# Kernel tuning notes

Hardware: AMD Instinct MI355X
Metric: run time of the kernel (lower is better)

## Reference

```python
import jax, jax.numpy as jnp
import numpy as np

E = 8        # num_experts
C = 1024     # n_emb
H = 4096     # n_emb * ff_mult
B, T = 4, 1024


def setup_inputs() -> dict:
    key = jax.random.key(0)
    k_x, k_g, k_1, k_2, k_3 = jax.random.split(key, 5)
    scale = 0.02
    return {
        "x": jax.random.normal(k_x, (B, T, C), dtype=jnp.float32),
        "Wg": jax.random.normal(k_g, (E, C), dtype=jnp.float32) * scale,   # gate: Linear(C, E), weight [E, C]
        "W1": jax.random.normal(k_1, (E, C, H), dtype=jnp.float32) * scale,  # per-expert w1 (transposed for einsum)
        "W2": jax.random.normal(k_2, (E, H, C), dtype=jnp.float32) * scale,  # per-expert w2
        "W3": jax.random.normal(k_3, (E, C, H), dtype=jnp.float32) * scale,  # per-expert w3
        "top_k": 2,
    }


def reference(x, Wg, W1, W2, W3, top_k):
    Bd, Td, Cd = x.shape
    xf = x.reshape(-1, Cd)                                   # [N, C]
    N = xf.shape[0]
    logits = jnp.einsum('nc,ec->ne', xf, Wg)                 # router logits [N, E]
    probs = jax.nn.softmax(logits.astype(jnp.float32), axis=-1)
    w, sel = jax.lax.top_k(probs, top_k)                     # [N, k]
    w = w / w.sum(axis=-1, keepdims=True)                    # renormalize over selected
    # combine weight per (token, expert): sum of normalized topk weights routed to e
    cw = jnp.zeros((N, E), jnp.float32).at[jnp.arange(N)[:, None], sel].add(w)
    # dense grouped SwiGLU over all experts; combine weights zero out unselected experts
    h1 = jnp.einsum('nc,ech->neh', xf, W1)                   # [N, E, H]
    g = jax.nn.silu(h1) * jnp.einsum('nc,ech->neh', xf, W3)  # [N, E, H]
    out = jnp.einsum('neh,ehc,ne->nc', g, W2, cw.astype(x.dtype))
    return out.reshape(Bd, Td, Cd)
```

## Files before the change

kernel.cpp:

```cpp
#include <hip/hip_runtime.h>
#include <hip/hip_bf16.h>

#define E_     8
#define C_     1024
#define H_     4096
#define N_TOK  4096
#define TOPK   2
#define NSLOT  (N_TOK*TOPK)
#define SPAD   (NSLOT+256)

#define LPAD 40

typedef __attribute__((ext_vector_type(4))) float f32x4;
typedef __attribute__((ext_vector_type(8))) short short8;

__device__ __forceinline__ unsigned short f2bf(float f) {
    return __builtin_bit_cast(unsigned short, __float2bfloat16(f));
}

__device__ __forceinline__ void gload16(const void* g, const void* l) {
    __builtin_amdgcn_global_load_lds(
        (const __attribute__((address_space(1))) unsigned int*)g,
        (__attribute__((address_space(3))) unsigned int*)l, 16, 0, 0);
}

#define WAITVM_(n) asm volatile("s_waitcnt vmcnt(" #n ")" ::: "memory")
#define WAITVM(n) WAITVM_(n)

__global__ void router_kernel(const float* __restrict__ x, const float* __restrict__ Wg,
                              int* __restrict__ sel, float* __restrict__ wts) {
    int wave = (blockIdx.x * blockDim.x + threadIdx.x) >> 6;
    int lane = threadIdx.x & 63;
    if (wave >= N_TOK) return;
    const float* xr = x + (size_t)wave * C_;
    float acc[E_];
#pragma unroll
    for (int e = 0; e < E_; ++e) acc[e] = 0.f;
    for (int c = lane; c < C_; c += 64) {
        float xv = xr[c];
#pragma unroll
        for (int e = 0; e < E_; ++e) acc[e] += xv * Wg[e * C_ + c];
    }
#pragma unroll
    for (int e = 0; e < E_; ++e) {
#pragma unroll
        for (int off = 32; off > 0; off >>= 1) acc[e] += __shfl_xor(acc[e], off);
    }
    if (lane == 0) {
        float mx = acc[0];
#pragma unroll
        for (int e = 1; e < E_; ++e) mx = fmaxf(mx, acc[e]);
        float p[E_]; float s = 0.f;
#pragma unroll
        for (int e = 0; e < E_; ++e) { p[e] = __expf(acc[e] - mx); s += p[e]; }
        float inv = 1.f / s;
#pragma unroll
        for (int e = 0; e < E_; ++e) p[e] *= inv;
        int b0 = 0; float v0 = p[0];
#pragma unroll
        for (int e = 1; e < E_; ++e) if (p[e] > v0) { v0 = p[e]; b0 = e; }
        int b1 = -1; float v1 = -1.f;
#pragma unroll
        for (int e = 0; e < E_; ++e) { if (e != b0 && p[e] > v1) { v1 = p[e]; b1 = e; } }
        float isum = 1.f / (v0 + v1);
        sel[wave*2]   = b0; sel[wave*2+1] = b1;
        wts[wave*2]   = v0 * isum; wts[wave*2+1] = v1 * isum;
    }
}

__global__ void assign_kernel(const int* __restrict__ sel, const float* __restrict__ wts,
                              int* __restrict__ counts, int* __restrict__ offsets,
                              int* __restrict__ pos_of_slot, int* __restrict__ token_of,
                              float* __restrict__ slotw) {
    __shared__ int cnt[256][E_];
    __shared__ int offs[E_];
    int t = threadIdx.x;
    const int PER = NSLOT / 256;
    int base = t * PER;
    int loc[E_];
#pragma unroll
    for (int e = 0; e < E_; ++e) loc[e] = 0;
    for (int i = 0; i < PER; ++i) loc[sel[base + i]]++;
#pragma unroll
    for (int e = 0; e < E_; ++e) cnt[t][e] = loc[e];
    __syncthreads();
    if (t < E_) {
        int run = 0;
        for (int i = 0; i < 256; ++i) { int c = cnt[i][t]; cnt[i][t] = run; run += c; }
        counts[t] = run;
    }
    __syncthreads();
    if (t == 0) {
        int s = 0;
        for (int e = 0; e < E_; ++e) { offs[e] = s; offsets[e] = s; s += counts[e]; }
    }
    __syncthreads();
    int run[E_];
#pragma unroll
    for (int e = 0; e < E_; ++e) run[e] = offs[e] + cnt[t][e];
    for (int i = 0; i < PER; ++i) {
        int s = base + i;
        int e = sel[s];
        int p = run[e]++;
        pos_of_slot[s] = p;
        token_of[p] = s >> 1;
        slotw[p] = wts[s];
    }
}

__global__ void copy_kernel(const float* __restrict__ x, const int* __restrict__ pos_of_slot,
                            unsigned short* __restrict__ Xg) {
    int slot = blockIdx.x * 4 + (threadIdx.x >> 6);
    int lane = threadIdx.x & 63;
    int pos = pos_of_slot[slot];
    int n = slot >> 1;
    const float* xr = x + (size_t)n * C_;
    unsigned short* dst = Xg + (size_t)pos * C_;
#pragma unroll
    for (int i = 0; i < 4; ++i) {
        int c0 = i * 256 + lane * 4;
        float4 v = *(const float4*)(xr + c0);
        ushort4 b;
        b.x = f2bf(v.x); b.y = f2bf(v.y); b.z = f2bf(v.z); b.w = f2bf(v.w);
        *(ushort4*)(dst + c0) = b;
    }
}

__global__ void wconv_kernel(const float* __restrict__ src, unsigned short* __restrict__ dst,
                             int R, int Cc) {
    int e = blockIdx.z;
    int c0 = blockIdx.x * 64;
    int r0 = blockIdx.y * 64;
    const float* s = src + (size_t)e * R * Cc;
    unsigned short* d = dst + (size_t)e * R * Cc;
    __shared__ unsigned short t_[64][72];
    int t = threadIdx.x;
    int tr = t >> 4, tc4 = (t & 15) * 4;
#pragma unroll
    for (int i = 0; i < 4; ++i) {
        int r = tr + i * 16;
        float4 v = *(const float4*)(s + (size_t)(r0 + r) * Cc + c0 + tc4);
        t_[r][tc4+0] = f2bf(v.x); t_[r][tc4+1] = f2bf(v.y);
        t_[r][tc4+2] = f2bf(v.z); t_[r][tc4+3] = f2bf(v.w);
    }
    __syncthreads();
    int oc = t >> 2, seg = (t & 3) * 16;
    short8 w0, w1;
#pragma unroll
    for (int j = 0; j < 8; ++j) {
        w0[j] = (short)t_[seg + j][oc];
        w1[j] = (short)t_[seg + 8 + j][oc];
    }
    unsigned short* dp = d + (size_t)(c0 + oc) * R + r0 + seg;
    *(short8*)dp = w0;
    *(short8*)(dp + 8) = w1;
}


#define G1_NH (C_/32)

__global__ __launch_bounds__(512, 2) void gemm1_ring(
        const unsigned short* __restrict__ Xg, const unsigned short* __restrict__ W1t,
        const unsigned short* __restrict__ W3t, unsigned short* __restrict__ G,
        const int* __restrict__ counts, const int* __restrict__ offsets) {
    int b = blockIdx.y * 32 + blockIdx.x;
    int e = b & 7;
    int j = b >> 3;
    int ct = j & 31;
    int rt = j >> 5;
    int ne = counts[e];
    if (rt * 256 >= ne) return;
    int row0 = offsets[e] + rt * 256;
    int n0 = ct * 128;

    extern __shared__ char lds[];
    char* As  = lds;
    char* B1s = lds + 65536;
    char* B3s = lds + 98304;

    int tid = threadIdx.x, lane = tid & 63, wid = tid >> 6;
    int wm = wid >> 1, wn = wid & 1;
    int fr = lane & 15, q = lane >> 4;
    int arow = lane & 15, akch = lane >> 4;

    const unsigned short* Ap  = Xg + (size_t)row0 * C_;
    const unsigned short* B1p = W1t + ((size_t)e * H_ + n0) * C_;
    const unsigned short* B3p = W3t + ((size_t)e * H_ + n0) * C_;

    f32x4 acc1[4][4], acc3[4][4];
#pragma unroll
    for (int m = 0; m < 4; ++m)
#pragma unroll
        for (int n = 0; n < 4; ++n) {
            acc1[m][n] = (f32x4){0.f,0.f,0.f,0.f};
            acc3[m][n] = (f32x4){0.f,0.f,0.f,0.f};
        }

    auto STAGE_A = [&](int hs, int slot) {
        int k0 = hs * 32;
#pragma unroll
        for (int jj = 0; jj < 2; ++jj) {
            int g = wid + jj * 8;
            gload16(Ap + (size_t)(g * 16 + arow) * C_ + k0 + akch * 8,
                    As + slot * 16384 + g * 1024);
        }
    };
    auto STAGE_B = [&](int hs, int slot) {
        int k0 = hs * 32;
        gload16(B1p + (size_t)(wid * 16 + arow) * C_ + k0 + akch * 8,
                B1s + slot * 8192 + wid * 1024);
        gload16(B3p + (size_t)(wid * 16 + arow) * C_ + k0 + akch * 8,
                B3s + slot * 8192 + wid * 1024);
    };

    STAGE_A(0, 0); STAGE_B(0, 0);
    STAGE_A(1, 1); STAGE_B(1, 1);
    STAGE_A(2, 2); STAGE_B(2, 2);
    WAITVM(8);
    __builtin_amdgcn_s_barrier();

    for (int h = 0; h < G1_NH; ++h) {
        int slot = h & 3;
        int hs = (h + 3 < G1_NH) ? h + 3 : G1_NH - 1;
        int wslot = (h + 3) & 3;
        short8 a[4], b1[4], b3[4];
#pragma unroll
        for (int m = 0; m < 4; ++m)
            a[m] = *(const short8*)(As + slot * 16384 + (wm * 4 + m) * 1024 + q * 256 + fr * 16);
#pragma unroll
        for (int n = 0; n < 4; ++n)
            b1[n] = *(const short8*)(B1s + slot * 8192 + (wn * 4 + n) * 1024 + q * 256 + fr * 16);
        STAGE_A(hs, wslot);
        __builtin_amdgcn_sched_barrier(0);
        __builtin_amdgcn_s_barrier();
        __builtin_amdgcn_s_setprio(1);
#pragma unroll
        for (int m = 0; m < 4; ++m)
#pragma unroll
            for (int n = 0; n < 4; ++n)
                acc1[m][n] = __builtin_amdgcn_mfma_f32_16x16x32_bf16(a[m], b1[n], acc1[m][n], 0, 0, 0);
        __builtin_amdgcn_s_setprio(0);
        __builtin_amdgcn_s_barrier();
#pragma unroll
        for (int n = 0; n < 4; ++n)
            b3[n] = *(const short8*)(B3s + slot * 8192 + (wn * 4 + n) * 1024 + q * 256 + fr * 16);
        STAGE_B(hs, wslot);
        WAITVM(8);
        __builtin_amdgcn_sched_barrier(0);
        __builtin_amdgcn_s_barrier();
        __builtin_amdgcn_s_setprio(1);
#pragma unroll
        for (int m = 0; m < 4; ++m)
#pragma unroll
            for (int n = 0; n < 4; ++n)
                acc3[m][n] = __builtin_amdgcn_mfma_f32_16x16x32_bf16(a[m], b3[n], acc3[m][n], 0, 0, 0);
        __builtin_amdgcn_s_setprio(0);
        __builtin_amdgcn_s_barrier();
    }
    WAITVM(0);

#pragma unroll
    for (int m = 0; m < 4; ++m)
#pragma unroll
        for (int rg = 0; rg < 4; ++rg) {
            int row = wm*64 + m*16 + q*4 + rg;
            if (rt * 256 + row < ne) {
                size_t gbase = (size_t)(row0 + row) * H_ + n0 + wn*64;
#pragma unroll
                for (int n = 0; n < 4; ++n) {
                    float h1 = acc1[m][n][rg];
                    float h3 = acc3[m][n][rg];
                    float g = h1 * h3 / (1.f + __expf(-h1));
                    G[gbase + n*16 + fr] = f2bf(g);
                }
            }
        }
}

#define G2_NH (H_/32)

__global__ __launch_bounds__(512, 2) void gemm2_ring(
        const unsigned short* __restrict__ G, const unsigned short* __restrict__ W2t,
        float* __restrict__ out, const int* __restrict__ counts,
        const int* __restrict__ offsets, const int* __restrict__ token_of,
        const float* __restrict__ slotw) {
    int b = blockIdx.y * 8 + blockIdx.x;
    int e = b & 7;
    int j = b >> 3;
    int ct = j & 7;
    int rt = j >> 3;
    int ne = counts[e];
    if (rt * 256 >= ne) return;
    int row0 = offsets[e] + rt * 256;
    int n0 = ct * 128;

    extern __shared__ char lds[];
    char* As = lds;
    char* Bs = lds + 98304;

    int tid = threadIdx.x, lane = tid & 63, wid = tid >> 6;
    int wm = wid >> 1, wn = wid & 1;
    int fr = lane & 15, q = lane >> 4;
    int arow = lane & 15, akch = lane >> 4;

    const unsigned short* Ap = G + (size_t)row0 * H_;
    const unsigned short* Bp = W2t + ((size_t)e * C_ + n0) * H_;

    f32x4 acc[4][4];
#pragma unroll
    for (int m = 0; m < 4; ++m)
#pragma unroll
        for (int n = 0; n < 4; ++n) acc[m][n] = (f32x4){0.f,0.f,0.f,0.f};

    auto STAGE = [&](int hs, int slot) {
        int k0 = hs * 32;
#pragma unroll
        for (int jj = 0; jj < 2; ++jj) {
            int g = wid + jj * 8;
            gload16(Ap + (size_t)(g * 16 + arow) * H_ + k0 + akch * 8,
                    As + slot * 16384 + g * 1024);
        }
        gload16(Bp + (size_t)(wid * 16 + arow) * H_ + k0 + akch * 8,
                Bs + slot * 8192 + wid * 1024);
    };

    STAGE(0, 0); STAGE(1, 1); STAGE(2, 2); STAGE(3, 3); STAGE(4, 4);
    WAITVM(12);
    __builtin_amdgcn_s_barrier();

    int slot = 0, wslot = 5;
    for (int h = 0; h < G2_NH; ++h) {
        int hs = (h + 5 < G2_NH) ? h + 5 : G2_NH - 1;
        short8 a[4], bfr[4];
#pragma unroll
        for (int m = 0; m < 4; ++m)
            a[m] = *(const short8*)(As + slot * 16384 + (wm * 4 + m) * 1024 + q * 256 + fr * 16);
#pragma unroll
        for (int n = 0; n < 4; ++n)
            bfr[n] = *(const short8*)(Bs + slot * 8192 + (wn * 4 + n) * 1024 + q * 256 + fr * 16);
        STAGE(hs, wslot);
        WAITVM(12);
        __builtin_amdgcn_sched_barrier(0);
        __builtin_amdgcn_s_barrier();
        __builtin_amdgcn_s_setprio(1);
#pragma unroll
        for (int m = 0; m < 4; ++m)
#pragma unroll
            for (int n = 0; n < 4; ++n)
                acc[m][n] = __builtin_amdgcn_mfma_f32_16x16x32_bf16(a[m], bfr[n], acc[m][n], 0, 0, 0);
        __builtin_amdgcn_s_setprio(0);
        __builtin_amdgcn_s_barrier();
        slot = (slot == 5) ? 0 : slot + 1;
        wslot = (wslot == 5) ? 0 : wslot + 1;
    }
    WAITVM(0);

#pragma unroll
    for (int m = 0; m < 4; ++m)
#pragma unroll
        for (int rg = 0; rg < 4; ++rg) {
            int row = wm*64 + m*16 + q*4 + rg;
            if (rt * 256 + row < ne) {
                int grow = row0 + row;
                int tok = token_of[grow];
                float w = slotw[grow];
                float* orow = out + (size_t)tok * C_ + n0 + wn*64;
#pragma unroll
                for (int n = 0; n < 4; ++n)
                    atomicAdd(orow + n*16 + fr, acc[m][n][rg] * w);
            }
        }
}

#define BM 128
#define BN 128
#define BK 32
__global__ __launch_bounds__(256, 2) void gemm1_slow(
        const unsigned short* __restrict__ Xg, const float* __restrict__ W1,
        const float* __restrict__ W3, unsigned short* __restrict__ G,
        const int* __restrict__ counts, const int* __restrict__ offsets) {
    int ct = blockIdx.x;
    int rslot = blockIdx.y;
    int e = rslot >> 5, rt = rslot & 31;
    int ne = counts[e];
    if (rt * BM >= ne) return;
    int row0 = offsets[e] + rt * BM;
    int n0 = ct * BN;

    __shared__ unsigned short As[BM][LPAD];
    __shared__ unsigned short B1s[BN][LPAD];
    __shared__ unsigned short B3s[BN][LPAD];

    int tid = threadIdx.x;
    int lane = tid & 63, wid = tid >> 6;
    int wr = (wid >> 1) * 64, wc = (wid & 1) * 64;

    f32x4 acc1[4][4], acc3[4][4];
#pragma unroll
    for (int m = 0; m < 4; ++m)
#pragma unroll
        for (int n = 0; n < 4; ++n) {
            acc1[m][n] = (f32x4){0.f,0.f,0.f,0.f};
            acc3[m][n] = (f32x4){0.f,0.f,0.f,0.f};
        }

    const float* B1p = W1 + (size_t)e * C_ * H_ + n0;
    const float* B3p = W3 + (size_t)e * C_ * H_ + n0;
    int chunk = tid & 3, rr = tid >> 2;
    int kq = tid >> 5, n4 = tid & 31;

    for (int k0 = 0; k0 < C_; k0 += BK) {
        __syncthreads();
#pragma unroll
        for (int h = 0; h < 2; ++h) {
            int row = rr + h * 64;
            uint4 v = *(const uint4*)(Xg + (size_t)(row0 + row) * C_ + k0 + chunk * 8);
            *(uint4*)&As[row][chunk * 8] = v;
        }
        {
            float4 r0 = *(const float4*)(B1p + (size_t)(k0 + kq*4 + 0) * H_ + n4*4);
            float4 r1 = *(const float4*)(B1p + (size_t)(k0 + kq*4 + 1) * H_ + n4*4);
            float4 r2 = *(const float4*)(B1p + (size_t)(k0 + kq*4 + 2) * H_ + n4*4);
            float4 r3 = *(const float4*)(B1p + (size_t)(k0 + kq*4 + 3) * H_ + n4*4);
            ushort4 w0 = {f2bf(r0.x), f2bf(r1.x), f2bf(r2.x), f2bf(r3.x)};
            ushort4 w1 = {f2bf(r0.y), f2bf(r1.y), f2bf(r2.y), f2bf(r3.y)};
            ushort4 w2 = {f2bf(r0.z), f2bf(r1.z), f2bf(r2.z), f2bf(r3.z)};
            ushort4 w3 = {f2bf(r0.w), f2bf(r1.w), f2bf(r2.w), f2bf(r3.w)};
            *(ushort4*)&B1s[n4*4+0][kq*4] = w0;
            *(ushort4*)&B1s[n4*4+1][kq*4] = w1;
            *(ushort4*)&B1s[n4*4+2][kq*4] = w2;
            *(ushort4*)&B1s[n4*4+3][kq*4] = w3;
            r0 = *(const float4*)(B3p + (size_t)(k0 + kq*4 + 0) * H_ + n4*4);
            r1 = *(const float4*)(B3p + (size_t)(k0 + kq*4 + 1) * H_ + n4*4);
            r2 = *(const float4*)(B3p + (size_t)(k0 + kq*4 + 2) * H_ + n4*4);
            r3 = *(const float4*)(B3p + (size_t)(k0 + kq*4 + 3) * H_ + n4*4);
            w0 = (ushort4){f2bf(r0.x), f2bf(r1.x), f2bf(r2.x), f2bf(r3.x)};
            w1 = (ushort4){f2bf(r0.y), f2bf(r1.y), f2bf(r2.y), f2bf(r3.y)};
            w2 = (ushort4){f2bf(r0.z), f2bf(r1.z), f2bf(r2.z), f2bf(r3.z)};
            w3 = (ushort4){f2bf(r0.w), f2bf(r1.w), f2bf(r2.w), f2bf(r3.w)};
            *(ushort4*)&B3s[n4*4+0][kq*4] = w0;
            *(ushort4*)&B3s[n4*4+1][kq*4] = w1;
            *(ushort4*)&B3s[n4*4+2][kq*4] = w2;
            *(ushort4*)&B3s[n4*4+3][kq*4] = w3;
        }
        __syncthreads();
        int q = lane >> 4, fr = lane & 15;
        short8 a[4], b1[4], b3[4];
#pragma unroll
        for (int m = 0; m < 4; ++m) a[m] = *(const short8*)&As[wr + m*16 + fr][q*8];
#pragma unroll
        for (int n = 0; n < 4; ++n) {
            b1[n] = *(const short8*)&B1s[wc + n*16 + fr][q*8];
            b3[n] = *(const short8*)&B3s[wc + n*16 + fr][q*8];
        }
#pragma unroll
        for (int m = 0; m < 4; ++m)
#pragma unroll
            for (int n = 0; n < 4; ++n) {
                acc1[m][n] = __builtin_amdgcn_mfma_f32_16x16x32_bf16(a[m], b1[n], acc1[m][n], 0, 0, 0);
                acc3[m][n] = __builtin_amdgcn_mfma_f32_16x16x32_bf16(a[m], b3[n], acc3[m][n], 0, 0, 0);
            }
    }
    int q = lane >> 4, cfr = lane & 15;
#pragma unroll
    for (int m = 0; m < 4; ++m) {
#pragma unroll
        for (int rg = 0; rg < 4; ++rg) {
            int row = wr + m*16 + q*4 + rg;
            if (rt * BM + row < ne) {
                size_t gbase = (size_t)(row0 + row) * H_ + n0;
#pragma unroll
                for (int n = 0; n < 4; ++n) {
                    float h1 = acc1[m][n][rg];
                    float h3 = acc3[m][n][rg];
                    float g = h1 * h3 / (1.f + __expf(-h1));
                    G[gbase + wc + n*16 + cfr] = f2bf(g);
                }
            }
        }
    }
}

__global__ __launch_bounds__(256, 2) void gemm2_slow(
        const unsigned short* __restrict__ G, const float* __restrict__ W2,
        float* __restrict__ out, const int* __restrict__ counts,
        const int* __restrict__ offsets, const int* __restrict__ token_of,
        const float* __restrict__ slotw) {
    int ct = blockIdx.x;
    int rslot = blockIdx.y;
    int e = rslot >> 5, rt = rslot & 31;
    int ne = counts[e];
    if (rt * BM >= ne) return;
    int row0 = offsets[e] + rt * BM;
    int n0 = ct * BN;

    __shared__ unsigned short As[BM][LPAD];
    __shared__ unsigned short Bs[BN][LPAD];

    int tid = threadIdx.x;
    int lane = tid & 63, wid = tid >> 6;
    int wr = (wid >> 1) * 64, wc = (wid & 1) * 64;

    f32x4 acc[4][4];
#pragma unroll
    for (int m = 0; m < 4; ++m)
#pragma unroll
        for (int n = 0; n < 4; ++n) acc[m][n] = (f32x4){0.f,0.f,0.f,0.f};

    const float* Bp = W2 + (size_t)e * H_ * C_ + n0;
    int chunk = tid & 3, rr = tid >> 2;
    int kq = tid >> 5, n4 = tid & 31;

    for (int k0 = 0; k0 < H_; k0 += BK) {
        __syncthreads();
#pragma unroll
        for (int h = 0; h < 2; ++h) {
            int row = rr + h * 64;
            uint4 v = *(const uint4*)(G + (size_t)(row0 + row) * H_ + k0 + chunk * 8);
            *(uint4*)&As[row][chunk * 8] = v;
        }
        {
            float4 r0 = *(const float4*)(Bp + (size_t)(k0 + kq*4 + 0) * C_ + n4*4);
            float4 r1 = *(const float4*)(Bp + (size_t)(k0 + kq*4 + 1) * C_ + n4*4);
            float4 r2 = *(const float4*)(Bp + (size_t)(k0 + kq*4 + 2) * C_ + n4*4);
            float4 r3 = *(const float4*)(Bp + (size_t)(k0 + kq*4 + 3) * C_ + n4*4);
            ushort4 w0 = {f2bf(r0.x), f2bf(r1.x), f2bf(r2.x), f2bf(r3.x)};
            ushort4 w1 = {f2bf(r0.y), f2bf(r1.y), f2bf(r2.y), f2bf(r3.y)};
            ushort4 w2 = {f2bf(r0.z), f2bf(r1.z), f2bf(r2.z), f2bf(r3.z)};
            ushort4 w3 = {f2bf(r0.w), f2bf(r1.w), f2bf(r2.w), f2bf(r3.w)};
            *(ushort4*)&Bs[n4*4+0][kq*4] = w0;
            *(ushort4*)&Bs[n4*4+1][kq*4] = w1;
            *(ushort4*)&Bs[n4*4+2][kq*4] = w2;
            *(ushort4*)&Bs[n4*4+3][kq*4] = w3;
        }
        __syncthreads();
        int q = lane >> 4, fr = lane & 15;
        short8 a[4], b[4];
#pragma unroll
        for (int m = 0; m < 4; ++m) a[m] = *(const short8*)&As[wr + m*16 + fr][q*8];
#pragma unroll
        for (int n = 0; n < 4; ++n) b[n] = *(const short8*)&Bs[wc + n*16 + fr][q*8];
#pragma unroll
        for (int m = 0; m < 4; ++m)
#pragma unroll
            for (int n = 0; n < 4; ++n)
                acc[m][n] = __builtin_amdgcn_mfma_f32_16x16x32_bf16(a[m], b[n], acc[m][n], 0, 0, 0);
    }
    int q = lane >> 4, cfr = lane & 15;
#pragma unroll
    for (int m = 0; m < 4; ++m) {
#pragma unroll
        for (int rg = 0; rg < 4; ++rg) {
            int row = wr + m*16 + q*4 + rg;
            if (rt * BM + row < ne) {
                int grow = row0 + row;
                int tok = token_of[grow];
                float w = slotw[grow];
                float* orow = out + (size_t)tok * C_ + n0;
#pragma unroll
                for (int n = 0; n < 4; ++n)
                    atomicAdd(orow + wc + n*16 + cfr, acc[m][n][rg] * w);
            }
        }
    }
}

extern "C" void kernel_launch(void* const* d_in, const int* in_sizes, int n_in,
                              void* d_out, int out_size, void* d_ws, size_t ws_size,
                              hipStream_t stream) {
    const float* x  = (const float*)d_in[0];
    const float* Wg = (const float*)d_in[1];
    const float* W1 = (const float*)d_in[2];
    const float* W2 = (const float*)d_in[3];
    const float* W3 = (const float*)d_in[4];
    float* out = (float*)d_out;

    char* ws = (char*)d_ws;
    size_t o = 0;
    int*   sel      = (int*)(ws + o);  o += (size_t)NSLOT * 4;
    float* wts      = (float*)(ws + o); o += (size_t)NSLOT * 4;
    int*   pos      = (int*)(ws + o);  o += (size_t)NSLOT * 4;
    int*   token_of = (int*)(ws + o);  o += (size_t)NSLOT * 4;
    float* slotw    = (float*)(ws + o); o += (size_t)NSLOT * 4;
    int*   counts   = (int*)(ws + o);
    int*   offsets  = counts + E_;     o += 256;
    unsigned short* Xg = (unsigned short*)(ws + o); o += (size_t)SPAD * C_ * 2;
    unsigned short* G  = (unsigned short*)(ws + o); o += (size_t)SPAD * H_ * 2;
    size_t need_slow = o;
    unsigned short* W1t = (unsigned short*)(ws + o); o += (size_t)E_ * H_ * C_ * 2;
    unsigned short* W3t = (unsigned short*)(ws + o); o += (size_t)E_ * H_ * C_ * 2;
    unsigned short* W2t = W1t;
    size_t need_fast = o;

    hipMemsetAsync(d_out, 0, (size_t)out_size * sizeof(float), stream);
    if (ws_size < need_slow) return;

    router_kernel<<<N_TOK/4, 256, 0, stream>>>(x, Wg, sel, wts);
    assign_kernel<<<1, 256, 0, stream>>>(sel, wts, counts, offsets, pos, token_of, slotw);
    copy_kernel<<<NSLOT/4, 256, 0, stream>>>(x, pos, Xg);

    if (ws_size >= need_fast) {
        hipFuncSetAttribute((const void*)gemm1_ring, hipFuncAttributeMaxDynamicSharedMemorySize, 131072);
        hipFuncSetAttribute((const void*)gemm2_ring, hipFuncAttributeMaxDynamicSharedMemorySize, 147456);
        wconv_kernel<<<dim3(H_/64, C_/64, E_), 256, 0, stream>>>(W1, W1t, C_, H_);
        wconv_kernel<<<dim3(H_/64, C_/64, E_), 256, 0, stream>>>(W3, W3t, C_, H_);
        gemm1_ring<<<dim3(H_/128, E_*32), 512, 131072, stream>>>(Xg, W1t, W3t, G, counts, offsets);
        wconv_kernel<<<dim3(C_/64, H_/64, E_), 256, 0, stream>>>(W2, W2t, H_, C_);
        gemm2_ring<<<dim3(C_/128, E_*32), 512, 147456, stream>>>(G, W2t, out, counts, offsets, token_of, slotw);
    } else {
        gemm1_slow<<<dim3(H_/BN, E_*32), 256, 0, stream>>>(Xg, W1, W3, G, counts, offsets);
        gemm2_slow<<<dim3(C_/BN, E_*32), 256, 0, stream>>>(G, W2, out, counts, offsets, token_of, slotw);
    }
}
```

Measured before the change: 594.4 us.

## Shrink expert GEMM tiles to 128x128 with 256 threads and shorter LDS rings

Both grouped expert GEMMs move from 256-row tiles with 512 threads to 128-row tiles with 256 threads (4 waves), which cuts LDS use and should let more blocks fit per CU. gemm1 merges its separate W1 and W3 stages into one stage per k-step with a 3-slot ring, and gemm2 shrinks from a 6-slot to a 4-slot ring. The aim is better occupancy and less padding waste on uneven per-expert token counts, at the cost of loading each weight tile twice as often and issuing more blocks.

```diff
diff --git a/kernel.cpp b/kernel.cpp
--- a/kernel.cpp
+++ b/kernel.cpp
@@ -159,7 +159,7 @@
 
 #define G1_NH (C_/32)
 
-__global__ __launch_bounds__(512, 2) void gemm1_ring(
+__global__ __launch_bounds__(256, 2) void gemm1_ring(
         const unsigned short* __restrict__ Xg, const unsigned short* __restrict__ W1t,
         const unsigned short* __restrict__ W3t, unsigned short* __restrict__ G,
         const int* __restrict__ counts, const int* __restrict__ offsets) {
@@ -169,14 +169,14 @@
     int ct = j & 31;
     int rt = j >> 5;
     int ne = counts[e];
-    if (rt * 256 >= ne) return;
-    int row0 = offsets[e] + rt * 256;
+    if (rt * 128 >= ne) return;
+    int row0 = offsets[e] + rt * 128;
     int n0 = ct * 128;
 
     extern __shared__ char lds[];
     char* As  = lds;
-    char* B1s = lds + 65536;
-    char* B3s = lds + 98304;
+    char* B1s = lds + 24576;
+    char* B3s = lds + 49152;
 
     int tid = threadIdx.x, lane = tid & 63, wid = tid >> 6;
     int wm = wid >> 1, wn = wid & 1;
@@ -196,66 +196,51 @@
             acc3[m][n] = (f32x4){0.f,0.f,0.f,0.f};
         }
 
-    auto STAGE_A = [&](int hs, int slot) {
+    auto STAGE = [&](int hs, int slot) {
         int k0 = hs * 32;
 #pragma unroll
         for (int jj = 0; jj < 2; ++jj) {
-            int g = wid + jj * 8;
-            gload16(Ap + (size_t)(g * 16 + arow) * C_ + k0 + akch * 8,
-                    As + slot * 16384 + g * 1024);
+            int g = wid + jj * 4;
+            gload16(Ap  + (size_t)(g * 16 + arow) * C_ + k0 + akch * 8,
+                    As  + slot * 8192 + g * 1024);
+            gload16(B1p + (size_t)(g * 16 + arow) * C_ + k0 + akch * 8,
+                    B1s + slot * 8192 + g * 1024);
+            gload16(B3p + (size_t)(g * 16 + arow) * C_ + k0 + akch * 8,
+                    B3s + slot * 8192 + g * 1024);
         }
     };
-    auto STAGE_B = [&](int hs, int slot) {
-        int k0 = hs * 32;
-        gload16(B1p + (size_t)(wid * 16 + arow) * C_ + k0 + akch * 8,
-                B1s + slot * 8192 + wid * 1024);
-        gload16(B3p + (size_t)(wid * 16 + arow) * C_ + k0 + akch * 8,
-                B3s + slot * 8192 + wid * 1024);
-    };
-
-    STAGE_A(0, 0); STAGE_B(0, 0);
-    STAGE_A(1, 1); STAGE_B(1, 1);
-    STAGE_A(2, 2); STAGE_B(2, 2);
-    WAITVM(8);
+
+    STAGE(0, 0); STAGE(1, 1);
+    WAITVM(6);
     __builtin_amdgcn_s_barrier();
 
     for (int h = 0; h < G1_NH; ++h) {
-        int slot = h & 3;
-        int hs = (h + 3 < G1_NH) ? h + 3 : G1_NH - 1;
-        int wslot = (h + 3) & 3;
+        int slot = h % 3;
+        int hs = (h + 2 < G1_NH) ? h + 2 : G1_NH - 1;
+        int wslot = (h + 2) % 3;
         short8 a[4], b1[4], b3[4];
 #pragma unroll
         for (int m = 0; m < 4; ++m)
-            a[m] = *(const short8*)(As + slot * 16384 + (wm * 4 + m) * 1024 + q * 256 + fr * 16);
-#pragma unroll
-        for (int n = 0; n < 4; ++n)
+            a[m] = *(const short8*)(As + slot * 8192 + (wm * 4 + m) * 1024 + q * 256 + fr * 16);
+#pragma unroll
+        for (int n = 0; n < 4; ++n) {
             b1[n] = *(const short8*)(B1s + slot * 8192 + (wn * 4 + n) * 1024 + q * 256 + fr * 16);
-        STAGE_A(hs, wslot);
+            b3[n] = *(const short8*)(B3s + slot * 8192 + (wn * 4 + n) * 1024 + q * 256 + fr * 16);
+        }
+        STAGE(hs, wslot);
+        WAITVM(6);
         __builtin_amdgcn_sched_barrier(0);
         __builtin_amdgcn_s_barrier();
         __builtin_amdgcn_s_setprio(1);
 #pragma unroll
         for (int m = 0; m < 4; ++m)
 #pragma unroll
-            for (int n = 0; n < 4; ++n)
+            for (int n = 0; n < 4; ++n) {
                 acc1[m][n] = __builtin_amdgcn_mfma_f32_16x16x32_bf16(a[m], b1[n], acc1[m][n], 0, 0, 0);
+                acc3[m][n] = __builtin_amdgcn_mfma_f32_16x16x32_bf16(a[m], b3[n], acc3[m][n], 0, 0, 0);
+            }
         __builtin_amdgcn_s_setprio(0);
         __builtin_amdgcn_s_barrier();
-#pragma unroll
-        for (int n = 0; n < 4; ++n)
-            b3[n] = *(const short8*)(B3s + slot * 8192 + (wn * 4 + n) * 1024 + q * 256 + fr * 16);
-        STAGE_B(hs, wslot);
-        WAITVM(8);
-        __builtin_amdgcn_sched_barrier(0);
-        __builtin_amdgcn_s_barrier();
-        __builtin_amdgcn_s_setprio(1);
-#pragma unroll
-        for (int m = 0; m < 4; ++m)
-#pragma unroll
-            for (int n = 0; n < 4; ++n)
-                acc3[m][n] = __builtin_amdgcn_mfma_f32_16x16x32_bf16(a[m], b3[n], acc3[m][n], 0, 0, 0);
-        __builtin_amdgcn_s_setprio(0);
-        __builtin_amdgcn_s_barrier();
     }
     WAITVM(0);
 
@@ -264,7 +249,7 @@
 #pragma unroll
         for (int rg = 0; rg < 4; ++rg) {
             int row = wm*64 + m*16 + q*4 + rg;
-            if (rt * 256 + row < ne) {
+            if (rt * 128 + row < ne) {
                 size_t gbase = (size_t)(row0 + row) * H_ + n0 + wn*64;
 #pragma unroll
                 for (int n = 0; n < 4; ++n) {
@@ -279,7 +264,7 @@
 
 #define G2_NH (H_/32)
 
-__global__ __launch_bounds__(512, 2) void gemm2_ring(
+__global__ __launch_bounds__(256, 2) void gemm2_ring(
         const unsigned short* __restrict__ G, const unsigned short* __restrict__ W2t,
         float* __restrict__ out, const int* __restrict__ counts,
         const int* __restrict__ offsets, const int* __restrict__ token_of,
@@ -290,13 +275,13 @@
     int ct = j & 7;
     int rt = j >> 3;
     int ne = counts[e];
-    if (rt * 256 >= ne) return;
-    int row0 = offsets[e] + rt * 256;
+    if (rt * 128 >= ne) return;
+    int row0 = offsets[e] + rt * 128;
     int n0 = ct * 128;
 
     extern __shared__ char lds[];
     char* As = lds;
-    char* Bs = lds + 98304;
+    char* Bs = lds + 32768;
 
     int tid = threadIdx.x, lane = tid & 63, wid = tid >> 6;
     int wm = wid >> 1, wn = wid & 1;
@@ -316,30 +301,30 @@
         int k0 = hs * 32;
 #pragma unroll
         for (int jj = 0; jj < 2; ++jj) {
-            int g = wid + jj * 8;
+            int g = wid + jj * 4;
             gload16(Ap + (size_t)(g * 16 + arow) * H_ + k0 + akch * 8,
-                    As + slot * 16384 + g * 1024);
-        }
-        gload16(Bp + (size_t)(wid * 16 + arow) * H_ + k0 + akch * 8,
-                Bs + slot * 8192 + wid * 1024);
+                    As + slot * 8192 + g * 1024);
+            gload16(Bp + (size_t)(g * 16 + arow) * H_ + k0 + akch * 8,
+                    Bs + slot * 8192 + g * 1024);
+        }
     };
 
-    STAGE(0, 0); STAGE(1, 1); STAGE(2, 2); STAGE(3, 3); STAGE(4, 4);
-    WAITVM(12);
+    STAGE(0, 0); STAGE(1, 1); STAGE(2, 2);
+    WAITVM(8);
     __builtin_amdgcn_s_barrier();
 
-    int slot = 0, wslot = 5;
     for (int h = 0; h < G2_NH; ++h) {
-        int hs = (h + 5 < G2_NH) ? h + 5 : G2_NH - 1;
+        int slot = h & 3;
+        int hs = (h + 3 < G2_NH) ? h + 3 : G2_NH - 1;
         short8 a[4], bfr[4];
 #pragma unroll
         for (int m = 0; m < 4; ++m)
-            a[m] = *(const short8*)(As + slot * 16384 + (wm * 4 + m) * 1024 + q * 256 + fr * 16);
+            a[m] = *(const short8*)(As + slot * 8192 + (wm * 4 + m) * 1024 + q * 256 + fr * 16);
 #pragma unroll
         for (int n = 0; n < 4; ++n)
             bfr[n] = *(const short8*)(Bs + slot * 8192 + (wn * 4 + n) * 1024 + q * 256 + fr * 16);
-        STAGE(hs, wslot);
-        WAITVM(12);
+        STAGE(hs, (h + 3) & 3);
+        WAITVM(8);
         __builtin_amdgcn_sched_barrier(0);
         __builtin_amdgcn_s_barrier();
         __builtin_amdgcn_s_setprio(1);
@@ -350,8 +335,6 @@
                 acc[m][n] = __builtin_amdgcn_mfma_f32_16x16x32_bf16(a[m], bfr[n], acc[m][n], 0, 0, 0);
         __builtin_amdgcn_s_setprio(0);
         __builtin_amdgcn_s_barrier();
-        slot = (slot == 5) ? 0 : slot + 1;
-        wslot = (wslot == 5) ? 0 : wslot + 1;
     }
     WAITVM(0);
 
@@ -360,7 +343,7 @@
 #pragma unroll
         for (int rg = 0; rg < 4; ++rg) {
             int row = wm*64 + m*16 + q*4 + rg;
-            if (rt * 256 + row < ne) {
+            if (rt * 128 + row < ne) {
                 int grow = row0 + row;
                 int tok = token_of[grow];
                 float w = slotw[grow];
@@ -600,13 +583,13 @@
     copy_kernel<<<NSLOT/4, 256, 0, stream>>>(x, pos, Xg);
 
     if (ws_size >= need_fast) {
-        hipFuncSetAttribute((const void*)gemm1_ring, hipFuncAttributeMaxDynamicSharedMemorySize, 131072);
-        hipFuncSetAttribute((const void*)gemm2_ring, hipFuncAttributeMaxDynamicSharedMemorySize, 147456);
+        hipFuncSetAttribute((const void*)gemm1_ring, hipFuncAttributeMaxDynamicSharedMemorySize, 73728);
+        hipFuncSetAttribute((const void*)gemm2_ring, hipFuncAttributeMaxDynamicSharedMemorySize, 65536);
         wconv_kernel<<<dim3(H_/64, C_/64, E_), 256, 0, stream>>>(W1, W1t, C_, H_);
         wconv_kernel<<<dim3(H_/64, C_/64, E_), 256, 0, stream>>>(W3, W3t, C_, H_);
-        gemm1_ring<<<dim3(H_/128, E_*32), 512, 131072, stream>>>(Xg, W1t, W3t, G, counts, offsets);
+        gemm1_ring<<<dim3(32, 256), 256, 73728, stream>>>(Xg, W1t, W3t, G, counts, offsets);
         wconv_kernel<<<dim3(C_/64, H_/64, E_), 256, 0, stream>>>(W2, W2t, H_, C_);
-        gemm2_ring<<<dim3(C_/128, E_*32), 512, 147456, stream>>>(G, W2t, out, counts, offsets, token_of, slotw);
+        gemm2_ring<<<dim3(8, 256), 256, 65536, stream>>>(G, W2t, out, counts, offsets, token_of, slotw);
     } else {
         gemm1_slow<<<dim3(H_/BN, E_*32), 256, 0, stream>>>(Xg, W1, W3, G, counts, offsets);
         gemm2_slow<<<dim3(C_/BN, E_*32), 256, 0, stream>>>(G, W2, out, counts, offsets, token_of, slotw);
```

Result: no change. 589.9 us (-0.8%).

## Restructure GEMM ring pipelines to single barrier per k-step with 4-buffer ring

Applied to the files above, without the earlier changes.

Both grouped GEMM kernels move from a deeper prefetch ring with two barriers per k-step to a 4-slot ring with prefetch distance 2 and one barrier per iteration. Loads are issued before the wait, and the B1/B3 fragments in gemm1 share one register array. gemm2 LDS drops from 144KB to 96KB, which may allow more resident blocks, at the cost of less latency hiding from the shallower prefetch. A-tile row assignment per wave also changes. Relying on a distance-2 lookahead with 4 buffers is what avoids a WAR race after the barriers are removed.

```diff
diff --git a/kernel.cpp b/kernel.cpp
--- a/kernel.cpp
+++ b/kernel.cpp
@@ -157,7 +157,7 @@
 }
 
 
-#define G1_NH (C_/32)
+#define G1_NT (C_/32)
 
 __global__ __launch_bounds__(512, 2) void gemm1_ring(
         const unsigned short* __restrict__ Xg, const unsigned short* __restrict__ W1t,
@@ -196,66 +196,52 @@
             acc3[m][n] = (f32x4){0.f,0.f,0.f,0.f};
         }
 
-    auto STAGE_A = [&](int hs, int slot) {
-        int k0 = hs * 32;
+    auto STAGE = [&](int ts, int buf) {
+        int k0 = ts * 32;
 #pragma unroll
         for (int jj = 0; jj < 2; ++jj) {
-            int g = wid + jj * 8;
-            gload16(Ap + (size_t)(g * 16 + arow) * C_ + k0 + akch * 8,
-                    As + slot * 16384 + g * 1024);
-        }
+            int ab = wid * 2 + jj;
+            gload16(Ap + (size_t)(ab * 16 + arow) * C_ + k0 + akch * 8,
+                    As + buf * 16384 + ab * 1024);
+        }
+        gload16(B1p + (size_t)(wid * 16 + arow) * C_ + k0 + akch * 8,
+                B1s + buf * 8192 + wid * 1024);
+        gload16(B3p + (size_t)(wid * 16 + arow) * C_ + k0 + akch * 8,
+                B3s + buf * 8192 + wid * 1024);
     };
-    auto STAGE_B = [&](int hs, int slot) {
-        int k0 = hs * 32;
-        gload16(B1p + (size_t)(wid * 16 + arow) * C_ + k0 + akch * 8,
-                B1s + slot * 8192 + wid * 1024);
-        gload16(B3p + (size_t)(wid * 16 + arow) * C_ + k0 + akch * 8,
-                B3s + slot * 8192 + wid * 1024);
-    };
-
-    STAGE_A(0, 0); STAGE_B(0, 0);
-    STAGE_A(1, 1); STAGE_B(1, 1);
-    STAGE_A(2, 2); STAGE_B(2, 2);
-    WAITVM(8);
-    __builtin_amdgcn_s_barrier();
-
-    for (int h = 0; h < G1_NH; ++h) {
-        int slot = h & 3;
-        int hs = (h + 3 < G1_NH) ? h + 3 : G1_NH - 1;
-        int wslot = (h + 3) & 3;
-        short8 a[4], b1[4], b3[4];
-#pragma unroll
-        for (int m = 0; m < 4; ++m)
-            a[m] = *(const short8*)(As + slot * 16384 + (wm * 4 + m) * 1024 + q * 256 + fr * 16);
+
+    STAGE(0, 0); STAGE(1, 1);
+    for (int t = 0; t < G1_NT; ++t) {
+        int ts = (t + 2 < G1_NT) ? t + 2 : G1_NT - 1;
+        STAGE(ts, (t + 2) & 3);
+        WAITVM(8);
+        __builtin_amdgcn_s_barrier();
+        __builtin_amdgcn_sched_barrier(0);
+        int buf = t & 3;
+        short8 a[4], bb[4];
+#pragma unroll
+        for (int m = 0; m < 4; ++m)
+            a[m] = *(const short8*)(As + buf * 16384 + (wm * 4 + m) * 1024 + q * 256 + fr * 16);
 #pragma unroll
         for (int n = 0; n < 4; ++n)
-            b1[n] = *(const short8*)(B1s + slot * 8192 + (wn * 4 + n) * 1024 + q * 256 + fr * 16);
-        STAGE_A(hs, wslot);
-        __builtin_amdgcn_sched_barrier(0);
-        __builtin_amdgcn_s_barrier();
+            bb[n] = *(const short8*)(B1s + buf * 8192 + (wn * 4 + n) * 1024 + q * 256 + fr * 16);
         __builtin_amdgcn_s_setprio(1);
 #pragma unroll
         for (int m = 0; m < 4; ++m)
 #pragma unroll
             for (int n = 0; n < 4; ++n)
-                acc1[m][n] = __builtin_amdgcn_mfma_f32_16x16x32_bf16(a[m], b1[n], acc1[m][n], 0, 0, 0);
+                acc1[m][n] = __builtin_amdgcn_mfma_f32_16x16x32_bf16(a[m], bb[n], acc1[m][n], 0, 0, 0);
         __builtin_amdgcn_s_setprio(0);
-        __builtin_amdgcn_s_barrier();
 #pragma unroll
         for (int n = 0; n < 4; ++n)
-            b3[n] = *(const short8*)(B3s + slot * 8192 + (wn * 4 + n) * 1024 + q * 256 + fr * 16);
-        STAGE_B(hs, wslot);
-        WAITVM(8);
-        __builtin_amdgcn_sched_barrier(0);
-        __builtin_amdgcn_s_barrier();
+            bb[n] = *(const short8*)(B3s + buf * 8192 + (wn * 4 + n) * 1024 + q * 256 + fr * 16);
         __builtin_amdgcn_s_setprio(1);
 #pragma unroll
         for (int m = 0; m < 4; ++m)
 #pragma unroll
             for (int n = 0; n < 4; ++n)
-                acc3[m][n] = __builtin_amdgcn_mfma_f32_16x16x32_bf16(a[m], b3[n], acc3[m][n], 0, 0, 0);
+                acc3[m][n] = __builtin_amdgcn_mfma_f32_16x16x32_bf16(a[m], bb[n], acc3[m][n], 0, 0, 0);
         __builtin_amdgcn_s_setprio(0);
-        __builtin_amdgcn_s_barrier();
     }
     WAITVM(0);
 
@@ -277,7 +263,7 @@
         }
 }
 
-#define G2_NH (H_/32)
+#define G2_NT (H_/32)
 
 __global__ __launch_bounds__(512, 2) void gemm2_ring(
         const unsigned short* __restrict__ G, const unsigned short* __restrict__ W2t,
@@ -296,7 +282,7 @@
 
     extern __shared__ char lds[];
     char* As = lds;
-    char* Bs = lds + 98304;
+    char* Bs = lds + 65536;
 
     int tid = threadIdx.x, lane = tid & 63, wid = tid >> 6;
     int wm = wid >> 1, wn = wid & 1;
@@ -312,46 +298,40 @@
 #pragma unroll
         for (int n = 0; n < 4; ++n) acc[m][n] = (f32x4){0.f,0.f,0.f,0.f};
 
-    auto STAGE = [&](int hs, int slot) {
-        int k0 = hs * 32;
+    auto STAGE = [&](int ts, int buf) {
+        int k0 = ts * 32;
 #pragma unroll
         for (int jj = 0; jj < 2; ++jj) {
-            int g = wid + jj * 8;
-            gload16(Ap + (size_t)(g * 16 + arow) * H_ + k0 + akch * 8,
-                    As + slot * 16384 + g * 1024);
+            int ab = wid * 2 + jj;
+            gload16(Ap + (size_t)(ab * 16 + arow) * H_ + k0 + akch * 8,
+                    As + buf * 16384 + ab * 1024);
         }
         gload16(Bp + (size_t)(wid * 16 + arow) * H_ + k0 + akch * 8,
-                Bs + slot * 8192 + wid * 1024);
+                Bs + buf * 8192 + wid * 1024);
     };
 
-    STAGE(0, 0); STAGE(1, 1); STAGE(2, 2); STAGE(3, 3); STAGE(4, 4);
-    WAITVM(12);
-    __builtin_amdgcn_s_barrier();
-
-    int slot = 0, wslot = 5;
-    for (int h = 0; h < G2_NH; ++h) {
-        int hs = (h + 5 < G2_NH) ? h + 5 : G2_NH - 1;
-        short8 a[4], bfr[4];
-#pragma unroll
-        for (int m = 0; m < 4; ++m)
-            a[m] = *(const short8*)(As + slot * 16384 + (wm * 4 + m) * 1024 + q * 256 + fr * 16);
+    STAGE(0, 0); STAGE(1, 1);
+    for (int t = 0; t < G2_NT; ++t) {
+        int ts = (t + 2 < G2_NT) ? t + 2 : G2_NT - 1;
+        STAGE(ts, (t + 2) & 3);
+        WAITVM(6);
+        __builtin_amdgcn_s_barrier();
+        __builtin_amdgcn_sched_barrier(0);
+        int buf = t & 3;
+        short8 a[4], bb[4];
+#pragma unroll
+        for (int m = 0; m < 4; ++m)
+            a[m] = *(const short8*)(As + buf * 16384 + (wm * 4 + m) * 1024 + q * 256 + fr * 16);
 #pragma unroll
         for (int n = 0; n < 4; ++n)
-            bfr[n] = *(const short8*)(Bs + slot * 8192 + (wn * 4 + n) * 1024 + q * 256 + fr * 16);
-        STAGE(hs, wslot);
-        WAITVM(12);
-        __builtin_amdgcn_sched_barrier(0);
-        __builtin_amdgcn_s_barrier();
+            bb[n] = *(const short8*)(Bs + buf * 8192 + (wn * 4 + n) * 1024 + q * 256 + fr * 16);
         __builtin_amdgcn_s_setprio(1);
 #pragma unroll
         for (int m = 0; m < 4; ++m)
 #pragma unroll
             for (int n = 0; n < 4; ++n)
-                acc[m][n] = __builtin_amdgcn_mfma_f32_16x16x32_bf16(a[m], bfr[n], acc[m][n], 0, 0, 0);
+                acc[m][n] = __builtin_amdgcn_mfma_f32_16x16x32_bf16(a[m], bb[n], acc[m][n], 0, 0, 0);
         __builtin_amdgcn_s_setprio(0);
-        __builtin_amdgcn_s_barrier();
-        slot = (slot == 5) ? 0 : slot + 1;
-        wslot = (wslot == 5) ? 0 : wslot + 1;
     }
     WAITVM(0);
 
@@ -601,12 +581,12 @@
 
     if (ws_size >= need_fast) {
         hipFuncSetAttribute((const void*)gemm1_ring, hipFuncAttributeMaxDynamicSharedMemorySize, 131072);
-        hipFuncSetAttribute((const void*)gemm2_ring, hipFuncAttributeMaxDynamicSharedMemorySize, 147456);
+        hipFuncSetAttribute((const void*)gemm2_ring, hipFuncAttributeMaxDynamicSharedMemorySize, 98304);
         wconv_kernel<<<dim3(H_/64, C_/64, E_), 256, 0, stream>>>(W1, W1t, C_, H_);
         wconv_kernel<<<dim3(H_/64, C_/64, E_), 256, 0, stream>>>(W3, W3t, C_, H_);
-        gemm1_ring<<<dim3(H_/128, E_*32), 512, 131072, stream>>>(Xg, W1t, W3t, G, counts, offsets);
+        gemm1_ring<<<dim3(32, 256), 512, 131072, stream>>>(Xg, W1t, W3t, G, counts, offsets);
         wconv_kernel<<<dim3(C_/64, H_/64, E_), 256, 0, stream>>>(W2, W2t, H_, C_);
-        gemm2_ring<<<dim3(C_/128, E_*32), 512, 147456, stream>>>(G, W2t, out, counts, offsets, token_of, slotw);
+        gemm2_ring<<<dim3(8, 256), 512, 98304, stream>>>(G, W2t, out, counts, offsets, token_of, slotw);
     } else {
         gemm1_slow<<<dim3(H_/BN, E_*32), 256, 0, stream>>>(Xg, W1, W3, G, counts, offsets);
         gemm2_slow<<<dim3(C_/BN, E_*32), 256, 0, stream>>>(G, W2, out, counts, offsets, token_of, slotw);
```

Result: no change. 585.0 us (-1.6%).
